# Optimization experiments

Measured on AMD Instinct MI355X. Metric: run time of the kernel, lower is better.

Reference implementation:

```python
import jax, jax.numpy as jnp
import numpy as np

D_MODEL = 1024
N_HEADS = 16
HEAD_DIM = D_MODEL // N_HEADS
B, T = 4, 2048


def setup_inputs() -> dict:
    key = jax.random.key(0)
    k1, k2, k3, k4 = jax.random.split(key, 4)
    x = jax.random.normal(k1, (B, T, D_MODEL), dtype=jnp.float32)
    # bool key-padding mask: True = masked (padded) position
    pad_mask = jax.random.randint(k2, (B, T), 0, 2).astype(jnp.bool_)
    # torch Linear weights: [out_features, in_features], bias=False
    W_qkv = jax.random.normal(k3, (3 * D_MODEL, D_MODEL), dtype=jnp.float32) * (1.0 / np.sqrt(D_MODEL))
    W_proj = jax.random.normal(k4, (D_MODEL, D_MODEL), dtype=jnp.float32) * (1.0 / np.sqrt(D_MODEL))
    return {"x": x, "pad_mask": pad_mask, "W_qkv": W_qkv, "W_proj": W_proj}


def reference(x, pad_mask, W_qkv, W_proj):
    Bv, Tv, C = x.shape
    H, Dh = N_HEADS, HEAD_DIM
    # qkv projection: x @ W_qkv.T -> [B,T,3C], reshape to [B,T,3,H,Dh]
    qkv = jnp.einsum('btc,oc->bto', x, W_qkv).reshape(Bv, Tv, 3, H, Dh)
    q = jnp.transpose(qkv[:, :, 0], (0, 2, 1, 3))  # [B,H,T,Dh]
    k = jnp.transpose(qkv[:, :, 1], (0, 2, 1, 3))
    v = jnp.transpose(qkv[:, :, 2], (0, 2, 1, 3))
    scale = 1.0 / jnp.sqrt(jnp.asarray(Dh, x.dtype))
    attn = jnp.einsum('bhqd,bhkd->bhqk', q, k) * scale  # [B,H,T,T]
    # key-padding mask: broadcast [B,1,1,T]
    attn = jnp.where(pad_mask[:, None, None, :], -jnp.inf, attn)
    attn = jax.nn.softmax(attn, axis=-1)
    out = jnp.einsum('bhqk,bhkd->bhqd', attn, v)  # [B,H,T,Dh]
    out = jnp.transpose(out, (0, 2, 1, 3)).reshape(Bv, Tv, C)
    return jnp.einsum('btc,oc->bto', out, W_proj)
```

## Files before the change

### kernel.cpp

```cpp
#include <hip/hip_runtime.h>
#include <hip/hip_bf16.h>
#include <stdint.h>

typedef __bf16 bf16_t;
typedef __bf16 bf16x8 __attribute__((ext_vector_type(8)));
typedef __bf16 bf16x4 __attribute__((ext_vector_type(4)));
typedef float f32x4 __attribute__((ext_vector_type(4)));

#define DEVFN static __device__ __forceinline__

DEVFN f32x4 mfma16(bf16x8 a, bf16x8 b, f32x4 c) {
  return __builtin_amdgcn_mfma_f32_16x16x32_bf16(a, b, c, 0, 0, 0);
}

#define GLL16(gsrc, ldst) __builtin_amdgcn_global_load_lds( \
    (__attribute__((address_space(1))) void*)(gsrc), \
    (__attribute__((address_space(3))) void*)(ldst), 16, 0, 0)

#define SCALE_Q 0.1803368801111204f

__global__ void cvt_all(const float* __restrict__ x, const float* __restrict__ wqkv,
                        const float* __restrict__ wproj, bf16_t* __restrict__ xb,
                        bf16_t* __restrict__ wqkvb, bf16_t* __restrict__ wprojb) {
  const int i = blockIdx.x * 256 + threadIdx.x;
  const float* s;
  bf16_t* d;
  int off;
  if (i < 2097152) { s = x; d = xb; off = i; }
  else if (i < 2097152 + 786432) { s = wqkv; d = wqkvb; off = i - 2097152; }
  else { s = wproj; d = wprojb; off = i - 2883584; }
  f32x4 v = reinterpret_cast<const f32x4*>(s)[off];
  bf16x4 o;
  o[0] = (bf16_t)v[0]; o[1] = (bf16_t)v[1]; o[2] = (bf16_t)v[2]; o[3] = (bf16_t)v[3];
  reinterpret_cast<bf16x4*>(d)[off] = o;
}

__global__ void build_idx(const int* __restrict__ mask, int* __restrict__ tc,
                          int* __restrict__ nk, bf16_t* __restrict__ kb,
                          bf16_t* __restrict__ vtb) {
  const int b = blockIdx.x;
  const int tid = threadIdx.x;
  const int lane = tid & 63, wv = tid >> 6;
  __shared__ int nk_s;
  const int* mrow = mask + b * 2048;
  if (wv == 0) {
    int base = 0;
    for (int cs = 0; cs < 2048; cs += 64) {
      const int mval = mrow[cs + lane];
      const unsigned long long bal = __ballot(mval == 0);
      const int pre = __popcll(bal & ((1ull << lane) - 1ull));
      if (!mval) tc[b * 2048 + base + pre] = cs + lane;
      base += __popcll(bal);
    }
    if (lane == 0) nk_s = base;
  }
  __syncthreads();
  const int nkb = nk_s;
  if (tid == 0) nk[b] = nkb;
  for (int i = nkb + tid; i < 2048; i += 256) tc[b * 2048 + i] = -1;
  const int ce = (nkb + 63) & ~63;
  for (int hh = wv; hh < 16; hh += 4) {
    const size_t bh = (size_t)(b * 16 + hh);
    for (int r = nkb; r < ce; ++r) {
      kb[(bh * 2048 + r) * 64 + lane] = (bf16_t)0.f;
      vtb[(bh * 64 + lane) * 2048 + r] = (bf16_t)0.f;
    }
  }
}

template <int EPI>
__global__ __launch_bounds__(256, 2)
void gemm_ct(const bf16_t* __restrict__ A, const bf16_t* __restrict__ Bx,
             bf16_t* __restrict__ qb, bf16_t* __restrict__ kb,
             bf16_t* __restrict__ vtb, float* __restrict__ fout,
             const int* __restrict__ tc, const int* __restrict__ nkp) {
  constexpr int K = 1024;
  __shared__ alignas(16) unsigned short At[128 * 64];
  __shared__ alignas(16) unsigned short Bt[128 * 64];
  const int tid = threadIdx.x;
  const int lane = tid & 63, w = tid >> 6;
  const int c = lane & 15, g = lane >> 4;
  const int oBase = blockIdx.x * 128, mBase = blockIdx.y * 128;
  const int wo = (w >> 1) * 64, wm = (w & 1) * 64;

  int nkb = 0;
  bool kv = false;
  if (EPI == 0) {
    nkb = nkp[mBase >> 11];
    kv = (blockIdx.x >= 8);
    if (kv && (mBase & 2047) >= nkb) return;
  }
  int brow[4];
#pragma unroll
  for (int i = 0; i < 4; ++i) {
    const int r = (i * 4 + w) * 8 + (lane >> 3);
    if (EPI == 0 && kv) {
      const int t = tc[(mBase >> 11) * 2048 + (mBase & 2047) + r];
      brow[i] = (mBase & ~2047) + (t < 0 ? 0 : t);
    } else {
      brow[i] = mBase + r;
    }
  }

  f32x4 acc[4][4] = {};

  for (int k0 = 0; k0 < K; k0 += 64) {
#pragma unroll
    for (int i = 0; i < 4; ++i) {
      const int cid = (i * 4 + w) * 64 + lane;
      const int r = cid >> 3;
      const int ss = (cid & 7) ^ (r & 7);
      GLL16(A + (size_t)(oBase + r) * K + k0 + ss * 8, &At[(i * 4 + w) * 512]);
      GLL16(Bx + (size_t)brow[i] * K + k0 + ss * 8, &Bt[(i * 4 + w) * 512]);
    }
    __syncthreads();
    bf16x8 af[4][2], bfr[4][2];
#pragma unroll
    for (int f = 0; f < 4; ++f) {
#pragma unroll
      for (int kc = 0; kc < 2; ++kc) {
        const int ra = wo + f * 16 + c;
        af[f][kc] = *reinterpret_cast<const bf16x8*>(&At[ra * 64 + ((kc * 4 + g) ^ (ra & 7)) * 8]);
        const int rb = wm + f * 16 + c;
        bfr[f][kc] = *reinterpret_cast<const bf16x8*>(&Bt[rb * 64 + ((kc * 4 + g) ^ (rb & 7)) * 8]);
      }
    }
    __builtin_amdgcn_s_setprio(1);
#pragma unroll
    for (int of = 0; of < 4; ++of)
#pragma unroll
      for (int mf = 0; mf < 4; ++mf)
#pragma unroll
        for (int kc = 0; kc < 2; ++kc)
          acc[of][mf] = mfma16(af[of][kc], bfr[mf][kc], acc[of][mf]);
    __builtin_amdgcn_s_setprio(0);
    __syncthreads();
  }

#pragma unroll
  for (int of = 0; of < 4; ++of) {
    const int o0 = oBase + wo + of * 16 + g * 4;
#pragma unroll
    for (int mf = 0; mf < 4; ++mf) {
      const int m = mBase + wm + mf * 16 + c;
      f32x4 v = acc[of][mf];
      if (EPI == 0) {
        if (!kv) {
          v[0] *= SCALE_Q; v[1] *= SCALE_Q; v[2] *= SCALE_Q; v[3] *= SCALE_Q;
          bf16x4 bv;
          bv[0] = (bf16_t)v[0]; bv[1] = (bf16_t)v[1]; bv[2] = (bf16_t)v[2]; bv[3] = (bf16_t)v[3];
          const int rem = o0 & 1023;
          const int h = rem >> 6, d0 = rem & 63;
          const int b = m >> 11, t = m & 2047;
          *reinterpret_cast<bf16x4*>(qb + (((size_t)(b * 16 + h)) * 2048 + t) * 64 + d0) = bv;
        } else {
          const int i = m & 2047;
          if (i < nkb) {
            bf16x4 bv;
            bv[0] = (bf16_t)v[0]; bv[1] = (bf16_t)v[1]; bv[2] = (bf16_t)v[2]; bv[3] = (bf16_t)v[3];
            const int rem = o0 & 1023;
            const int h = rem >> 6, d0 = rem & 63;
            const int b = m >> 11;
            const size_t bh = (size_t)(b * 16 + h);
            if (blockIdx.x < 16) {
              *reinterpret_cast<bf16x4*>(kb + (bh * 2048 + i) * 64 + d0) = bv;
            } else {
#pragma unroll
              for (int j = 0; j < 4; ++j)
                vtb[(bh * 64 + d0 + j) * 2048 + i] = bv[j];
            }
          }
        }
      } else {
        *reinterpret_cast<f32x4*>(fout + (size_t)m * 1024 + o0) = v;
      }
    }
  }
}

__global__ __launch_bounds__(256, 4)
void attn_fwd(const bf16_t* __restrict__ Qg, const bf16_t* __restrict__ Kg,
              const bf16_t* __restrict__ Vtg, const int* __restrict__ nkp,
              bf16_t* __restrict__ aout) {
  constexpr int T = 2048;
  __shared__ alignas(16) unsigned short KtL[2][64 * 64];
  __shared__ alignas(16) unsigned short VtL[2][64 * 64];
  const int tid = threadIdx.x, lane = tid & 63, w = tid >> 6;
  const int c = lane & 15, g = lane >> 4;
  const int bh = blockIdx.y, b = bh >> 4, h = bh & 15;
  const bf16_t* Qh = Qg + (size_t)bh * T * 64;
  const bf16_t* Kh = Kg + (size_t)bh * T * 64;
  const bf16_t* Vh = Vtg + (size_t)bh * 64 * T;
  const int q0 = blockIdx.x * 128 + w * 32;
  const int nkb = nkp[b];
  const int ntiles = (nkb + 63) >> 6;

  bf16x8 qfr[2][2];
#pragma unroll
  for (int qq = 0; qq < 2; ++qq)
#pragma unroll
    for (int dc = 0; dc < 2; ++dc)
      qfr[qq][dc] = *reinterpret_cast<const bf16x8*>(
          Qh + (size_t)(q0 + qq * 16 + c) * 64 + dc * 32 + g * 8);

  bf16x8 ones;
#pragma unroll
  for (int i = 0; i < 8; ++i) ones[i] = (bf16_t)1.0f;

  f32x4 oacc[4][2] = {};
  float lrun[2] = {0.f, 0.f};

  auto stage = [&](int t, int bi) {
    const int kt0 = t * 64;
#pragma unroll
    for (int i = 0; i < 2; ++i) {
      const int cid = (i * 4 + w) * 64 + lane;
      const int r = cid >> 3, p = cid & 7;
      const int lk = p ^ ((r & 3) | (((r >> 3) & 1) << 2));
      GLL16(Kh + (size_t)(kt0 + r) * 64 + lk * 8, &KtL[bi][(i * 4 + w) * 512]);
      const int lv = p ^ (r & 7);
      GLL16(Vh + (size_t)r * T + kt0 + lv * 8, &VtL[bi][(i * 4 + w) * 512]);
    }
  };

  stage(0, 0);
  __syncthreads();

  const int fK = (c & 3) | (((c >> 2) & 1) << 2);

  for (int t = 0; t < ntiles; ++t) {
    const int cur = t & 1;
    if (t + 1 < ntiles) stage(t + 1, cur ^ 1);

    bf16x8 kfr[4][2];
#pragma unroll
    for (int kr = 0; kr < 4; ++kr) {
      const int row = (c >> 2) * 8 + (kr & 1) * 4 + (c & 3) + (kr >> 1) * 32;
#pragma unroll
      for (int dc = 0; dc < 2; ++dc)
        kfr[kr][dc] = *reinterpret_cast<const bf16x8*>(
            &KtL[cur][row * 64 + (((dc * 4 + g) ^ fK) * 8)]);
    }

    f32x4 st[4][2];
    const bool tail = (t == ntiles - 1) && (nkb & 63) != 0;
    __builtin_amdgcn_s_setprio(1);
    if (!tail) {
#pragma unroll
      for (int kr = 0; kr < 4; ++kr)
#pragma unroll
        for (int qq = 0; qq < 2; ++qq) {
          f32x4 z = {0.f, 0.f, 0.f, 0.f};
          z = mfma16(kfr[kr][0], qfr[qq][0], z);
          st[kr][qq] = mfma16(kfr[kr][1], qfr[qq][1], z);
        }
    } else {
      const int ktk = t * 64;
#pragma unroll
      for (int kr = 0; kr < 4; ++kr) {
        const int kbase = ktk + g * 8 + (kr & 1) * 4 + (kr >> 1) * 32;
        f32x4 bias4;
#pragma unroll
        for (int j = 0; j < 4; ++j) bias4[j] = (kbase + j < nkb) ? 0.f : -1e30f;
#pragma unroll
        for (int qq = 0; qq < 2; ++qq) {
          f32x4 z = mfma16(kfr[kr][0], qfr[qq][0], bias4);
          st[kr][qq] = mfma16(kfr[kr][1], qfr[qq][1], z);
        }
      }
    }
    __builtin_amdgcn_s_setprio(0);

    bf16x8 pfr[2][2];
#pragma unroll
    for (int qq = 0; qq < 2; ++qq) {
#pragma unroll
      for (int kc = 0; kc < 2; ++kc) {
        bf16x8 p;
#pragma unroll
        for (int j = 0; j < 4; ++j) {
          p[j]     = (bf16_t)__builtin_amdgcn_exp2f(st[kc * 2 + 0][qq][j]);
          p[4 + j] = (bf16_t)__builtin_amdgcn_exp2f(st[kc * 2 + 1][qq][j]);
        }
        pfr[qq][kc] = p;
      }
      f32x4 su = {0.f, 0.f, 0.f, 0.f};
      su = mfma16(ones, pfr[qq][0], su);
      su = mfma16(ones, pfr[qq][1], su);
      lrun[qq] += su[0];
    }

    __builtin_amdgcn_s_setprio(1);
#pragma unroll
    for (int df = 0; df < 4; ++df) {
      bf16x8 va[2];
#pragma unroll
      for (int kc = 0; kc < 2; ++kc) {
        const int r = df * 16 + c;
        va[kc] = *reinterpret_cast<const bf16x8*>(
            &VtL[cur][r * 64 + ((kc * 4 + g) ^ (r & 7)) * 8]);
      }
#pragma unroll
      for (int qq = 0; qq < 2; ++qq)
#pragma unroll
        for (int kc = 0; kc < 2; ++kc)
          oacc[df][qq] = mfma16(va[kc], pfr[qq][kc], oacc[df][qq]);
    }
    __builtin_amdgcn_s_setprio(0);
    __syncthreads();
  }

#pragma unroll
  for (int qq = 0; qq < 2; ++qq) {
    const float inv = 1.0f / lrun[qq];
    const int q = q0 + qq * 16 + c;
#pragma unroll
    for (int df = 0; df < 4; ++df) {
      bf16x4 bv;
#pragma unroll
      for (int j = 0; j < 4; ++j) bv[j] = (bf16_t)(oacc[df][qq][j] * inv);
      const int d0 = df * 16 + g * 4;
      *reinterpret_cast<bf16x4*>(aout + ((size_t)(b * 2048 + q)) * 1024 + h * 64 + d0) = bv;
    }
  }
}

extern "C" void kernel_launch(void* const* d_in, const int* in_sizes, int n_in,
                              void* d_out, int out_size, void* d_ws, size_t ws_size,
                              hipStream_t stream) {
  (void)in_sizes; (void)n_in; (void)out_size; (void)ws_size;
  const float* x = (const float*)d_in[0];
  const int* pmask = (const int*)d_in[1];
  const float* wqkv = (const float*)d_in[2];
  const float* wproj = (const float*)d_in[3];
  float* out = (float*)d_out;
  char* ws = (char*)d_ws;

  bf16_t* xb    = (bf16_t*)(ws + 0);
  bf16_t* aob   = (bf16_t*)(ws + 0);
  bf16_t* wqkvb = (bf16_t*)(ws + 16777216);
  bf16_t* wprojb= (bf16_t*)(ws + 23068672);
  bf16_t* Qb    = (bf16_t*)(ws + 25165824);
  bf16_t* Kb    = (bf16_t*)(ws + 41943040);
  bf16_t* Vtb   = (bf16_t*)(ws + 58720256);

  int* tc  = (int*)d_out;
  int* nkp = tc + 4 * 2048;

  cvt_all<<<12288, 256, 0, stream>>>(x, wqkv, wproj, xb, wqkvb, wprojb);
  build_idx<<<4, 256, 0, stream>>>(pmask, tc, nkp, Kb, Vtb);

  gemm_ct<0><<<dim3(24, 64), 256, 0, stream>>>(wqkvb, xb, Qb, Kb, Vtb, nullptr, tc, nkp);
  attn_fwd<<<dim3(16, 64), 256, 0, stream>>>(Qb, Kb, Vtb, nkp, aob);
  gemm_ct<1><<<dim3(8, 64), 256, 0, stream>>>(wprojb, aob, nullptr, nullptr, nullptr, out,
                                              nullptr, nullptr);
}
```

Measured before the change: 158.4 us.

## Remap grids for XCD locality and double per-warp query rows in attention

Both GEMMs and the attention kernel now run on 1D grids whose block index is decoded so that blocks sharing the same M rows or the same batch-head land on the same XCD, which should improve L2 reuse of K/V and input tiles. The attention kernel now has each warp handle 64 query rows instead of 32, so every block covers 256 queries and each K/V tile staged in LDS is reused across twice as many rows. The score computation is reorganised per query group with a precomputed bias vector, so the non-tail path also adds a zero bias. Register pressure rises with the larger accumulators, so the occupancy hint drops from 4 to 2 blocks per CU.

Measured after the change: 151.1 us. 1.05x faster.

```diff
diff --git a/kernel.cpp b/kernel.cpp
--- a/kernel.cpp
+++ b/kernel.cpp
@@ -80,14 +80,18 @@
   const int tid = threadIdx.x;
   const int lane = tid & 63, w = tid >> 6;
   const int c = lane & 15, g = lane >> 4;
-  const int oBase = blockIdx.x * 128, mBase = blockIdx.y * 128;
+  const int bid = blockIdx.x;
+  const int xcd = bid & 7, jj = bid >> 3;
+  const int my = xcd * 8 + (jj & 7);
+  const int bx = jj >> 3;
+  const int oBase = bx * 128, mBase = my * 128;
   const int wo = (w >> 1) * 64, wm = (w & 1) * 64;
 
   int nkb = 0;
   bool kv = false;
   if (EPI == 0) {
     nkb = nkp[mBase >> 11];
-    kv = (blockIdx.x >= 8);
+    kv = (bx >= 8);
     if (kv && (mBase & 2047) >= nkb) return;
   }
   int brow[4];
@@ -162,7 +166,7 @@
             const int h = rem >> 6, d0 = rem & 63;
             const int b = m >> 11;
             const size_t bh = (size_t)(b * 16 + h);
-            if (blockIdx.x < 16) {
+            if (bx < 16) {
               *reinterpret_cast<bf16x4*>(kb + (bh * 2048 + i) * 64 + d0) = bv;
             } else {
 #pragma unroll
@@ -178,7 +182,7 @@
   }
 }
 
-__global__ __launch_bounds__(256, 4)
+__global__ __launch_bounds__(256, 2)
 void attn_fwd(const bf16_t* __restrict__ Qg, const bf16_t* __restrict__ Kg,
               const bf16_t* __restrict__ Vtg, const int* __restrict__ nkp,
               bf16_t* __restrict__ aout) {
@@ -187,17 +191,20 @@
   __shared__ alignas(16) unsigned short VtL[2][64 * 64];
   const int tid = threadIdx.x, lane = tid & 63, w = tid >> 6;
   const int c = lane & 15, g = lane >> 4;
-  const int bh = blockIdx.y, b = bh >> 4, h = bh & 15;
+  const int bid = blockIdx.x;
+  const int xcd = bid & 7, jj = bid >> 3;
+  const int bh = xcd * 8 + (jj & 7), qp = jj >> 3;
+  const int b = bh >> 4, h = bh & 15;
   const bf16_t* Qh = Qg + (size_t)bh * T * 64;
   const bf16_t* Kh = Kg + (size_t)bh * T * 64;
   const bf16_t* Vh = Vtg + (size_t)bh * 64 * T;
-  const int q0 = blockIdx.x * 128 + w * 32;
+  const int q0 = qp * 256 + w * 64;
   const int nkb = nkp[b];
   const int ntiles = (nkb + 63) >> 6;
 
-  bf16x8 qfr[2][2];
-#pragma unroll
-  for (int qq = 0; qq < 2; ++qq)
+  bf16x8 qfr[4][2];
+#pragma unroll
+  for (int qq = 0; qq < 4; ++qq)
 #pragma unroll
     for (int dc = 0; dc < 2; ++dc)
       qfr[qq][dc] = *reinterpret_cast<const bf16x8*>(
@@ -207,8 +214,8 @@
 #pragma unroll
   for (int i = 0; i < 8; ++i) ones[i] = (bf16_t)1.0f;
 
-  f32x4 oacc[4][2] = {};
-  float lrun[2] = {0.f, 0.f};
+  f32x4 oacc[4][4] = {};
+  float lrun[4] = {0.f, 0.f, 0.f, 0.f};
 
   auto stage = [&](int t, int bi) {
     const int kt0 = t * 64;
@@ -242,45 +249,37 @@
             &KtL[cur][row * 64 + (((dc * 4 + g) ^ fK) * 8)]);
     }
 
-    f32x4 st[4][2];
     const bool tail = (t == ntiles - 1) && (nkb & 63) != 0;
-    __builtin_amdgcn_s_setprio(1);
-    if (!tail) {
-#pragma unroll
-      for (int kr = 0; kr < 4; ++kr)
-#pragma unroll
-        for (int qq = 0; qq < 2; ++qq) {
-          f32x4 z = {0.f, 0.f, 0.f, 0.f};
-          z = mfma16(kfr[kr][0], qfr[qq][0], z);
-          st[kr][qq] = mfma16(kfr[kr][1], qfr[qq][1], z);
-        }
-    } else {
-      const int ktk = t * 64;
+    f32x4 bias4[4];
+#pragma unroll
+    for (int kr = 0; kr < 4; ++kr) {
+      if (tail) {
+        const int kbase = t * 64 + g * 8 + (kr & 1) * 4 + (kr >> 1) * 32;
+#pragma unroll
+        for (int j = 0; j < 4; ++j) bias4[kr][j] = (kbase + j < nkb) ? 0.f : -1e30f;
+      } else {
+        bias4[kr][0] = bias4[kr][1] = bias4[kr][2] = bias4[kr][3] = 0.f;
+      }
+    }
+
+    bf16x8 pfr[4][2];
+#pragma unroll
+    for (int qq = 0; qq < 4; ++qq) {
+      f32x4 stq[4];
+      __builtin_amdgcn_s_setprio(1);
 #pragma unroll
       for (int kr = 0; kr < 4; ++kr) {
-        const int kbase = ktk + g * 8 + (kr & 1) * 4 + (kr >> 1) * 32;
-        f32x4 bias4;
-#pragma unroll
-        for (int j = 0; j < 4; ++j) bias4[j] = (kbase + j < nkb) ? 0.f : -1e30f;
-#pragma unroll
-        for (int qq = 0; qq < 2; ++qq) {
-          f32x4 z = mfma16(kfr[kr][0], qfr[qq][0], bias4);
-          st[kr][qq] = mfma16(kfr[kr][1], qfr[qq][1], z);
-        }
-      }
-    }
-    __builtin_amdgcn_s_setprio(0);
-
-    bf16x8 pfr[2][2];
-#pragma unroll
-    for (int qq = 0; qq < 2; ++qq) {
+        f32x4 z = mfma16(kfr[kr][0], qfr[qq][0], bias4[kr]);
+        stq[kr] = mfma16(kfr[kr][1], qfr[qq][1], z);
+      }
+      __builtin_amdgcn_s_setprio(0);
 #pragma unroll
       for (int kc = 0; kc < 2; ++kc) {
         bf16x8 p;
 #pragma unroll
         for (int j = 0; j < 4; ++j) {
-          p[j]     = (bf16_t)__builtin_amdgcn_exp2f(st[kc * 2 + 0][qq][j]);
-          p[4 + j] = (bf16_t)__builtin_amdgcn_exp2f(st[kc * 2 + 1][qq][j]);
+          p[j]     = (bf16_t)__builtin_amdgcn_exp2f(stq[kc * 2 + 0][j]);
+          p[4 + j] = (bf16_t)__builtin_amdgcn_exp2f(stq[kc * 2 + 1][j]);
         }
         pfr[qq][kc] = p;
       }
@@ -301,7 +300,7 @@
             &VtL[cur][r * 64 + ((kc * 4 + g) ^ (r & 7)) * 8]);
       }
 #pragma unroll
-      for (int qq = 0; qq < 2; ++qq)
+      for (int qq = 0; qq < 4; ++qq)
 #pragma unroll
         for (int kc = 0; kc < 2; ++kc)
           oacc[df][qq] = mfma16(va[kc], pfr[qq][kc], oacc[df][qq]);
@@ -311,7 +310,7 @@
   }
 
 #pragma unroll
-  for (int qq = 0; qq < 2; ++qq) {
+  for (int qq = 0; qq < 4; ++qq) {
     const float inv = 1.0f / lrun[qq];
     const int q = q0 + qq * 16 + c;
 #pragma unroll
@@ -350,8 +349,8 @@
   cvt_all<<<12288, 256, 0, stream>>>(x, wqkv, wproj, xb, wqkvb, wprojb);
   build_idx<<<4, 256, 0, stream>>>(pmask, tc, nkp, Kb, Vtb);
 
-  gemm_ct<0><<<dim3(24, 64), 256, 0, stream>>>(wqkvb, xb, Qb, Kb, Vtb, nullptr, tc, nkp);
-  attn_fwd<<<dim3(16, 64), 256, 0, stream>>>(Qb, Kb, Vtb, nkp, aob);
-  gemm_ct<1><<<dim3(8, 64), 256, 0, stream>>>(wprojb, aob, nullptr, nullptr, nullptr, out,
-                                              nullptr, nullptr);
-}
+  gemm_ct<0><<<1536, 256, 0, stream>>>(wqkvb, xb, Qb, Kb, Vtb, nullptr, tc, nkp);
+  attn_fwd<<<512, 256, 0, stream>>>(Qb, Kb, Vtb, nkp, aob);
+  gemm_ct<1><<<512, 256, 0, stream>>>(wprojb, aob, nullptr, nullptr, nullptr, out,
+                                      nullptr, nullptr);
+}
```
